# Kernel tuning notes

Measured on AMD Instinct MI355X. Metric: run time of the kernel, lower is better.

Reference implementation:

```python
import jax, jax.numpy as jnp
import numpy as np
import math

D = 1024
H = 16
NEG = -10000.0


def _layernorm(x, g, b, eps=1e-6):
    mu = x.mean(-1, keepdims=True)
    var = ((x - mu) ** 2).mean(-1, keepdims=True)
    return (x - mu) / jnp.sqrt(var + eps) * g + b


def _gelu(x):
    return x * 0.5 * (1.0 + jax.lax.erf(x / math.sqrt(2.0)))


def _split_heads(x):
    N, L, _ = x.shape
    return x.reshape(N, L, H, D // H).transpose(0, 2, 1, 3)  # (N,H,L,d)


def _attention(q, k, v, mask):
    # q,k,v: (N,Lq/Lk,D); mask: (N,1,Lq,Lk) of 0/1 or None
    d = D // H
    qh, kh, vh = _split_heads(q), _split_heads(k), _split_heads(v)
    scores = jnp.einsum('bhqd,bhkd->bhqk', qh, kh) / math.sqrt(d)
    if mask is not None:
        scores = scores + (1.0 - mask) * NEG
    probs = jax.nn.softmax(scores, axis=-1)
    ctx = jnp.einsum('bhqk,bhkd->bhqd', probs, vh)
    N, _, Lq, _ = ctx.shape
    ctx = ctx.transpose(0, 2, 1, 3).reshape(N, Lq, D)
    return ctx, scores.mean(1)  # attention_vis = masked scaled scores averaged over heads


def setup_inputs() -> dict:
    key = jax.random.key(0)
    ks = jax.random.split(key, 16)
    N, Lt, Lv = 16, 512, 512
    w = lambda k: (jax.random.normal(k, (D, D), jnp.float32) * 0.02)
    inp = {
        'dec_hidden_states': jax.random.normal(ks[0], (N, Lt, D), jnp.float32),
        'dec_mask': jnp.ones((N, Lt), jnp.float32),
        'enc_outputs': jax.random.normal(ks[1], (N, Lv, D), jnp.float32),
        'sa_wq': w(ks[2]), 'sa_bq': jnp.zeros((D,), jnp.float32),
        'sa_wk': w(ks[3]), 'sa_bk': jnp.zeros((D,), jnp.float32),
        'sa_wv': w(ks[4]), 'sa_bv': jnp.zeros((D,), jnp.float32),
        'n1_g': jnp.ones((D,), jnp.float32), 'n1_b': jnp.zeros((D,), jnp.float32),
        'ca_wq': w(ks[5]), 'ca_bq': jnp.zeros((D,), jnp.float32),
        'ca_wk': w(ks[6]), 'ca_bk': jnp.zeros((D,), jnp.float32),
        'ca_wv': w(ks[7]), 'ca_bv': jnp.zeros((D,), jnp.float32),
        'n2_g': jnp.ones((D,), jnp.float32), 'n2_b': jnp.zeros((D,), jnp.float32),
        'int_w': w(ks[8]), 'int_b': jnp.zeros((D,), jnp.float32),
        'out_w': w(ks[9]), 'out_b': jnp.zeros((D,), jnp.float32),
        'out_g': jnp.ones((D,), jnp.float32), 'out_beta': jnp.zeros((D,), jnp.float32),
    }
    return inp


def reference(dec_hidden_states, dec_mask, enc_outputs,
              sa_wq, sa_bq, sa_wk, sa_bk, sa_wv, sa_bv, n1_g, n1_b,
              ca_wq, ca_bq, ca_wk, ca_bk, ca_wv, ca_bv, n2_g, n2_b,
              int_w, int_b, out_w, out_b, out_g, out_beta):
    x = dec_hidden_states
    N, Lt, _ = x.shape
    # causal + padding mask: (N,1,Lt) * tril(Lt,Lt) -> (N,Lt,Lt) -> (N,1,Lt,Lt)
    causal = jnp.tril(jnp.ones((Lt, Lt), x.dtype))
    self_mask = (dec_mask[:, None, :] * causal)[:, None, :, :]
    # self attention
    q = x @ sa_wq + sa_bq
    k = x @ sa_wk + sa_bk
    v = x @ sa_wv + sa_bv
    sa_ctx, _ = _attention(q, k, v, self_mask)
    h = _layernorm(sa_ctx + x, n1_g, n1_b)
    # cross attention (no mask)
    cq = h @ ca_wq + ca_bq
    ck = enc_outputs @ ca_wk + ca_bk
    cv = enc_outputs @ ca_wv + ca_bv
    ca_ctx, attention_vis = _attention(cq, ck, cv, None)
    h2 = _layernorm(h + ca_ctx, n2_g, n2_b)
    # intermediate (gelu FFN)
    inter = _gelu(h2 @ int_w + int_b)
    # Output: dense + residual(intermediate itself, as in original) + LayerNorm
    out = _layernorm(inter @ out_w + out_b + inter, out_g, out_beta)
    return out, attention_vis
```

## Files before the change

### kernel.cpp

```cpp
#include <hip/hip_runtime.h>
#include <hip/hip_bf16.h>
#include <math.h>

#define DDIM 1024
#define NH   16
#define LTOK 512
#define NBATCH 16

typedef unsigned short u16;
typedef unsigned short u16x8 __attribute__((ext_vector_type(8)));
typedef unsigned short u16x4 __attribute__((ext_vector_type(4)));
typedef __bf16 bf16x8 __attribute__((ext_vector_type(8)));
typedef float f32x4 __attribute__((ext_vector_type(4)));

typedef __attribute__((address_space(1))) void as1_void;
typedef __attribute__((address_space(3))) void as3_void;

__device__ __forceinline__ void llds16(const u16* g, u16* l) {
    __builtin_amdgcn_global_load_lds((as1_void*)g, (as3_void*)l, 16, 0, 0);
}

__device__ __forceinline__ float bf2f(u16 u) {
    unsigned v = ((unsigned)u) << 16;
    float f; __builtin_memcpy(&f, &v, 4); return f;
}
__device__ __forceinline__ u16 f2bf(float f) {
    unsigned u; __builtin_memcpy(&u, &f, 4);
    u += 0x7fffu + ((u >> 16) & 1u);
    return (u16)(u >> 16);
}

struct GemmOp {
    const u16* A; const u16* B; u16* C; float* Cf; const float* bias;
    u16* VTp;
    long sA1, sA2, sB1, sB2, sC1, sC2;
    int lda, ldb, ldc, M, N, K, zdiv, flags, nblk, vtcol0;
    float scale;
};

template<int MODE>
__global__ __launch_bounds__(256) void gemm_bt_kernel(GemmOp o1, GemmOp o2)
{
    constexpr int NB   = (MODE == 0) ? 1 : 2;
    constexpr int BUFE = 128 * 32;
    __shared__ __align__(16) u16 As[NB * BUFE];
    __shared__ __align__(16) u16 Bs[NB * BUFE];

    const bool second = (int)blockIdx.x >= o1.nblk;
    const GemmOp& o = second ? o2 : o1;
    int bidx = blockIdx.x - (second ? o1.nblk : 0);

    const int tilesN = o.N >> 7;
    const int tilesM = o.M >> 7;
    const int tiles  = tilesM * tilesN;
    const int z = bidx / tiles;
    const int t = bidx - z * tiles;
    const int zb = z / o.zdiv, zh = z - zb * o.zdiv;

    int tm, tn;
    if ((tilesM & 7) == 0) {
        const int xcd = t & 7, idx = t >> 3;
        const int mg  = tilesM >> 3;
        tm = ((idx % mg) << 3) | xcd;
        tn = idx / mg;
    } else {
        tm = t / tilesN;
        tn = t - tm * tilesN;
    }
    const int m0 = tm << 7, n0 = tn << 7;

    const u16* Ab = o.A + (long)zb * o.sA1 + (long)zh * o.sA2;
    const u16* Bb = o.B + (long)zb * o.sB1 + (long)zh * o.sB2;
    u16*   Cb  = o.C  ? o.C  + (long)zb * o.sC1 + (long)zh * o.sC2 : nullptr;
    float* Cfb = o.Cf ? o.Cf + (long)zb * o.sC1 + (long)zh * o.sC2 : nullptr;

    const int tid  = threadIdx.x;
    const int lane = tid & 63;
    const int wave = tid >> 6;
    const int wm = (wave & 1) << 6, wn = (wave >> 1) << 6;
    const int quad = lane >> 4, l16 = lane & 15;

    f32x4 acc[4][4];
#pragma unroll
    for (int i = 0; i < 4; i++)
#pragma unroll
        for (int j = 0; j < 4; j++) acc[i][j] = (f32x4){0.f, 0.f, 0.f, 0.f};

    const int lrA = (wave << 5) + (lane >> 2);
    const int lc  = (((lane & 3) ^ ((lane >> 3) & 3)) << 3);
    const u16* gA0 = Ab + (long)(m0 + lrA) * o.lda + lc;
    const u16* gA1 = Ab + (long)(m0 + lrA + 16) * o.lda + lc;
    const u16* gB0 = Bb + (long)(n0 + lrA) * o.ldb + lc;
    const u16* gB1 = Bb + (long)(n0 + lrA + 16) * o.ldb + lc;
    u16* lA0 = As + ((wave << 5) +  0) * 32;
    u16* lA1 = As + ((wave << 5) + 16) * 32;
    u16* lB0 = Bs + ((wave << 5) +  0) * 32;
    u16* lB1 = Bs + ((wave << 5) + 16) * 32;

    auto STAGE = [&](int bi, int k0) {
        llds16(gA0 + k0, lA0 + bi * BUFE);
        llds16(gA1 + k0, lA1 + bi * BUFE);
        llds16(gB0 + k0, lB0 + bi * BUFE);
        llds16(gB1 + k0, lB1 + bi * BUFE);
    };
    const int cadj = ((l16 >> 1) & 3) << 3;
    auto COMPUTE = [&](int bi) {
        const u16* Ac = As + bi * BUFE;
        const u16* Bc = Bs + bi * BUFE;
        bf16x8 af[4], bfr[4];
#pragma unroll
        for (int t2 = 0; t2 < 4; t2++)
            af[t2] = *(const bf16x8*)(Ac + (wm + t2 * 16 + l16) * 32
                                         + ((quad * 8) ^ cadj));
#pragma unroll
        for (int t2 = 0; t2 < 4; t2++)
            bfr[t2] = *(const bf16x8*)(Bc + (wn + t2 * 16 + l16) * 32
                                          + ((quad * 8) ^ cadj));
#pragma unroll
        for (int i = 0; i < 4; i++)
#pragma unroll
            for (int j = 0; j < 4; j++)
                acc[i][j] = __builtin_amdgcn_mfma_f32_16x16x32_bf16(
                    bfr[j], af[i], acc[i][j], 0, 0, 0);
    };

    const int K = o.K;
    if (MODE == 0) {
        for (int k0 = 0; k0 < K; k0 += 32) {
            __syncthreads();
            STAGE(0, k0);
            __syncthreads();
            COMPUTE(0);
        }
    } else {
        STAGE(0, 0);
        __syncthreads();
        int cur = 0;
        for (int k0 = 0; k0 < K; k0 += 32) {
            const int nxt = cur ^ 1;
            if (k0 + 32 < K) STAGE(nxt, k0 + 32);
            COMPUTE(cur);
            __syncthreads();
            cur = nxt;
        }
    }

#pragma unroll
    for (int i = 0; i < 4; i++) {
        const long row = m0 + wm + i * 16 + l16;
#pragma unroll
        for (int j = 0; j < 4; j++) {
            const int col = n0 + wn + j * 16 + quad * 4;
            f32x4 bv = o.bias ? *(const f32x4*)(o.bias + col)
                              : (f32x4){0.f, 0.f, 0.f, 0.f};
            f32x4 v4;
#pragma unroll
            for (int r = 0; r < 4; r++) {
                float v = acc[i][j][r] * o.scale + bv[r];
                if (o.flags & 1)
                    v = 0.5f * v * (1.f + erff(v * 0.70710678118654752f));
                v4[r] = v;
            }
            if (o.VTp && col >= o.vtcol0) {
                const int dv  = col - o.vtcol0;
                const long bh = (row >> 9) * NH + (dv >> 6);
                const int tok = (int)(row & (LTOK - 1));
                u16* vp = o.VTp + (bh * 64 + (dv & 63)) * LTOK + tok;
#pragma unroll
                for (int r = 0; r < 4; r++)
                    vp[(long)r * LTOK] = f2bf(v4[r]);
            } else if (Cfb) {
                *(f32x4*)(Cfb + row * o.ldc + col) = v4;
            } else {
                u16x4 ov;
#pragma unroll
                for (int r = 0; r < 4; r++) ov[r] = f2bf(v4[r]);
                *(u16x4*)(Cb + row * o.ldc + col) = ov;
            }
        }
    }
}

__global__ __launch_bounds__(256, 2) void flash_kernel(
    const u16* __restrict__ Q, const u16* __restrict__ K,
    const u16* __restrict__ VT, u16* __restrict__ O,
    const float* __restrict__ mask, int causal, int ldq, int ldk)
{
    __shared__ __align__(16) u16 Ks[128 * 72];
    __shared__ __align__(16) u16 Vs[64 * 136];
    const int tid  = threadIdx.x;
    const int wave = tid >> 6, lane = tid & 63;
    const int quad = lane >> 4, l16 = lane & 15;
    const int bh = blockIdx.x, qt = blockIdx.y, b = bh >> 4, h = bh & 15;
    const int qbase = qt * 128 + wave * 32;
    const int qrow0 = qbase + l16;
    const int qrow1 = qbase + 16 + l16;

    const u16* qp0 = Q + ((long)b * LTOK + qrow0) * ldq + h * 64 + quad * 8;
    const u16* qp1 = qp0 + (long)16 * ldq;
    bf16x8 aq00 = *(const bf16x8*)(qp0);
    bf16x8 aq01 = *(const bf16x8*)(qp0 + 32);
    bf16x8 aq10 = *(const bf16x8*)(qp1);
    bf16x8 aq11 = *(const bf16x8*)(qp1 + 32);

    f32x4 oacc0[4], oacc1[4];
#pragma unroll
    for (int jd = 0; jd < 4; jd++) {
        oacc0[jd] = (f32x4){0.f, 0.f, 0.f, 0.f};
        oacc1[jd] = (f32x4){0.f, 0.f, 0.f, 0.f};
    }
    float m0_ = -3.0e38f, m1_ = -3.0e38f;
    float l0_ = 0.f, l1_ = 0.f;

    const int krow = tid >> 3,       kcol = (tid & 7) << 3;
    const int vrow = tid >> 2,       vcol = (tid & 3) << 3;
    const u16* gK = K + ((long)b * LTOK + krow) * ldk + h * 64 + kcol;
    const u16* gV = VT + ((long)bh * 64 + vrow) * LTOK + vcol;

    const float C1    = 0.125f * 1.44269504088896340736f;
    const float NEGL2 = -10000.0f * 1.44269504088896340736f;

    const int nkt = causal ? (qt + 1) : (LTOK >> 7);

    u16x8 KR[4], VR[4];
#pragma unroll
    for (int i = 0; i < 4; i++) KR[i] = *(const u16x8*)(gK + (long)(i * 32) * ldk);
#pragma unroll
    for (int i = 0; i < 4; i++) VR[i] = *(const u16x8*)(gV + i * 32);
#pragma unroll
    for (int i = 0; i < 4; i++)
        *(u16x8*)(Ks + (i * 32 + krow) * 72 + kcol) = KR[i];
#pragma unroll
    for (int i = 0; i < 4; i++)
        *(u16x8*)(Vs + vrow * 136 + i * 32 + vcol) = VR[i];
    __syncthreads();

    for (int kt = 0; kt < nkt; kt++) {
        const int k0 = kt << 7;
        const bool more = (kt + 1 < nkt);

        if (more) {
            const int kn = k0 + 128;
#pragma unroll
            for (int i = 0; i < 4; i++)
                KR[i] = *(const u16x8*)(gK + (long)(kn + i * 32) * ldk);
#pragma unroll
            for (int i = 0; i < 4; i++)
                VR[i] = *(const u16x8*)(gV + kn + i * 32);
        }

        f32x4 s0[8], s1[8];
#pragma unroll
        for (int j = 0; j < 8; j++) {
            bf16x8 bk0 = *(const bf16x8*)(Ks + (j * 16 + l16) * 72 + quad * 8);
            bf16x8 bk1 = *(const bf16x8*)(Ks + (j * 16 + l16) * 72 + 32 + quad * 8);
            f32x4 z0 = (f32x4){0.f, 0.f, 0.f, 0.f};
            z0 = __builtin_amdgcn_mfma_f32_16x16x32_bf16(bk0, aq00, z0, 0, 0, 0);
            s0[j] = __builtin_amdgcn_mfma_f32_16x16x32_bf16(bk1, aq01, z0, 0, 0, 0);
            f32x4 z1 = (f32x4){0.f, 0.f, 0.f, 0.f};
            z1 = __builtin_amdgcn_mfma_f32_16x16x32_bf16(bk0, aq10, z1, 0, 0, 0);
            s1[j] = __builtin_amdgcn_mfma_f32_16x16x32_bf16(bk1, aq11, z1, 0, 0, 0);
        }

        float ta0 = -3.0e38f, ta1 = -3.0e38f, ta2 = -3.0e38f, ta3 = -3.0e38f;
        float tb0 = -3.0e38f, tb1 = -3.0e38f, tb2 = -3.0e38f, tb3 = -3.0e38f;
#pragma unroll
        for (int j = 0; j < 8; j++) {
            if (causal) {
                f32x4 m4 = *(const f32x4*)(mask + (long)b * LTOK + k0 + j * 16 + quad * 4);
#pragma unroll
                for (int r = 0; r < 4; r++) {
                    int key = k0 + j * 16 + quad * 4 + r;
                    float adm = fmaf(m4[r], -NEGL2, NEGL2);
                    s0[j][r] = fmaf(s0[j][r], C1, (key <= qrow0) ? adm : NEGL2);
                    s1[j][r] = fmaf(s1[j][r], C1, (key <= qrow1) ? adm : NEGL2);
                }
            } else {
#pragma unroll
                for (int r = 0; r < 4; r++) { s0[j][r] *= C1; s1[j][r] *= C1; }
            }
            ta0 = fmaxf(ta0, s0[j][0]); ta1 = fmaxf(ta1, s0[j][1]);
            ta2 = fmaxf(ta2, s0[j][2]); ta3 = fmaxf(ta3, s0[j][3]);
            tb0 = fmaxf(tb0, s1[j][0]); tb1 = fmaxf(tb1, s1[j][1]);
            tb2 = fmaxf(tb2, s1[j][2]); tb3 = fmaxf(tb3, s1[j][3]);
        }
        float tmax0 = fmaxf(fmaxf(ta0, ta1), fmaxf(ta2, ta3));
        float tmax1 = fmaxf(fmaxf(tb0, tb1), fmaxf(tb2, tb3));
        tmax0 = fmaxf(tmax0, __shfl_xor(tmax0, 16));
        tmax0 = fmaxf(tmax0, __shfl_xor(tmax0, 32));
        tmax1 = fmaxf(tmax1, __shfl_xor(tmax1, 16));
        tmax1 = fmaxf(tmax1, __shfl_xor(tmax1, 32));

        float mn0 = fmaxf(m0_, tmax0);
        float mn1 = fmaxf(m1_, tmax1);
        float al0 = __builtin_amdgcn_exp2f(m0_ - mn0);
        float al1 = __builtin_amdgcn_exp2f(m1_ - mn1);
        m0_ = mn0; m1_ = mn1;

        unsigned pk0[8][2], pk1[8][2];
        float ra0 = 0.f, ra1 = 0.f, ra2 = 0.f, ra3 = 0.f;
#pragma unroll
        for (int j = 0; j < 8; j++) {
            float p0 = __builtin_amdgcn_exp2f(s0[j][0] - mn0);
            float p1 = __builtin_amdgcn_exp2f(s0[j][1] - mn0);
            float p2 = __builtin_amdgcn_exp2f(s0[j][2] - mn0);
            float p3 = __builtin_amdgcn_exp2f(s0[j][3] - mn0);
            ra0 += p0; ra1 += p1; ra2 += p2; ra3 += p3;
            asm("v_cvt_pk_bf16_f32 %0, %1, %2" : "=v"(pk0[j][0]) : "v"(p0), "v"(p1));
            asm("v_cvt_pk_bf16_f32 %0, %1, %2" : "=v"(pk0[j][1]) : "v"(p2), "v"(p3));
        }
        float rsum0 = (ra0 + ra1) + (ra2 + ra3);
        float rb0 = 0.f, rb1 = 0.f, rb2 = 0.f, rb3 = 0.f;
#pragma unroll
        for (int j = 0; j < 8; j++) {
            float p0 = __builtin_amdgcn_exp2f(s1[j][0] - mn1);
            float p1 = __builtin_amdgcn_exp2f(s1[j][1] - mn1);
            float p2 = __builtin_amdgcn_exp2f(s1[j][2] - mn1);
            float p3 = __builtin_amdgcn_exp2f(s1[j][3] - mn1);
            rb0 += p0; rb1 += p1; rb2 += p2; rb3 += p3;
            asm("v_cvt_pk_bf16_f32 %0, %1, %2" : "=v"(pk1[j][0]) : "v"(p0), "v"(p1));
            asm("v_cvt_pk_bf16_f32 %0, %1, %2" : "=v"(pk1[j][1]) : "v"(p2), "v"(p3));
        }
        float rsum1 = (rb0 + rb1) + (rb2 + rb3);
        rsum0 += __shfl_xor(rsum0, 16);
        rsum0 += __shfl_xor(rsum0, 32);
        rsum1 += __shfl_xor(rsum1, 16);
        rsum1 += __shfl_xor(rsum1, 32);
        l0_ = l0_ * al0 + rsum0;
        l1_ = l1_ * al1 + rsum1;

#pragma unroll
        for (int jd = 0; jd < 4; jd++) { oacc0[jd] *= al0; oacc1[jd] *= al1; }

#pragma unroll
        for (int kk = 0; kk < 4; kk++) {
            unsigned wv0[4] = { pk0[2 * kk][0], pk0[2 * kk][1],
                                pk0[2 * kk + 1][0], pk0[2 * kk + 1][1] };
            unsigned wv1[4] = { pk1[2 * kk][0], pk1[2 * kk][1],
                                pk1[2 * kk + 1][0], pk1[2 * kk + 1][1] };
            bf16x8 bp0; __builtin_memcpy(&bp0, wv0, 16);
            bf16x8 bp1; __builtin_memcpy(&bp1, wv1, 16);
#pragma unroll
            for (int jd = 0; jd < 4; jd++) {
                const u16* vb = Vs + (jd * 16 + l16) * 136 + kk * 32 + quad * 4;
                u16 va[8];
                *(u16x4*)(va)     = *(const u16x4*)(vb);
                *(u16x4*)(va + 4) = *(const u16x4*)(vb + 16);
                bf16x8 av; __builtin_memcpy(&av, va, 16);
                oacc0[jd] = __builtin_amdgcn_mfma_f32_16x16x32_bf16(av, bp0, oacc0[jd], 0, 0, 0);
                oacc1[jd] = __builtin_amdgcn_mfma_f32_16x16x32_bf16(av, bp1, oacc1[jd], 0, 0, 0);
            }
        }

        if (more) {
            __syncthreads();
#pragma unroll
            for (int i = 0; i < 4; i++)
                *(u16x8*)(Ks + (i * 32 + krow) * 72 + kcol) = KR[i];
#pragma unroll
            for (int i = 0; i < 4; i++)
                *(u16x8*)(Vs + vrow * 136 + i * 32 + vcol) = VR[i];
            __syncthreads();
        }
    }

    float li0 = 1.f / l0_;
    float li1 = 1.f / l1_;
    long obase0 = ((long)b * LTOK + qrow0) * DDIM + h * 64;
    long obase1 = obase0 + (long)16 * DDIM;
#pragma unroll
    for (int jd = 0; jd < 4; jd++) {
        u16x4 ov0, ov1;
#pragma unroll
        for (int r = 0; r < 4; r++) {
            ov0[r] = f2bf(oacc0[jd][r] * li0);
            ov1[r] = f2bf(oacc1[jd][r] * li1);
        }
        *(u16x4*)(O + obase0 + jd * 16 + quad * 4) = ov0;
        *(u16x4*)(O + obase1 + jd * 16 + quad * 4) = ov1;
    }
}

__global__ __launch_bounds__(256) void add_ln_kernel(
    const u16* __restrict__ a, const u16* __restrict__ b,
    const float* __restrict__ b32,
    const float* __restrict__ g, const float* __restrict__ bt,
    u16* __restrict__ o, float* __restrict__ of)
{
    long row = blockIdx.x;
    int tid = threadIdx.x;
    __shared__ float red[4];
    const u16* ar = a + row * DDIM;
    float xv[4]; float s = 0.f;
#pragma unroll
    for (int i = 0; i < 4; i++) {
        int c = tid + 256 * i;
        float sum = bf2f(ar[c]) + (b32 ? b32[row * DDIM + c] : bf2f(b[row * DDIM + c]));
        xv[i] = fminf(fmaxf(sum, -1.0e18f), 1.0e18f);
        s += xv[i];
    }
#pragma unroll
    for (int ofs = 32; ofs >= 1; ofs >>= 1) s += __shfl_xor(s, ofs);
    int wave = tid >> 6, lane = tid & 63;
    if (lane == 0) red[wave] = s;
    __syncthreads();
    float mu = (red[0] + red[1] + red[2] + red[3]) * (1.f / 1024.f);
    __syncthreads();
    float v = 0.f;
#pragma unroll
    for (int i = 0; i < 4; i++) { float d = xv[i] - mu; v += d * d; }
#pragma unroll
    for (int ofs = 32; ofs >= 1; ofs >>= 1) v += __shfl_xor(v, ofs);
    if (lane == 0) red[wave] = v;
    __syncthreads();
    float var = (red[0] + red[1] + red[2] + red[3]) * (1.f / 1024.f);
    float inv = rsqrtf(var + 1e-6f);
#pragma unroll
    for (int i = 0; i < 4; i++) {
        int c = tid + 256 * i;
        float r = (xv[i] - mu) * inv * g[c] + bt[c];
        if (of) of[row * DDIM + c] = r;
        else    o [row * DDIM + c] = f2bf(r);
    }
}

__global__ __launch_bounds__(256) void cvt2_kernel(
    const float* __restrict__ s0, u16* __restrict__ d0,
    const float* __restrict__ s1, u16* __restrict__ d1)
{
    const float* src = blockIdx.y ? s1 : s0;
    u16* dst = blockIdx.y ? d1 : d0;
    long i = ((long)blockIdx.x * 256 + threadIdx.x) * 8;
    u16x8 o;
#pragma unroll
    for (int j = 0; j < 8; j++) o[j] = f2bf(src[i + j]);
    *(u16x8*)(dst + i) = o;
}

__global__ __launch_bounds__(256) void wt_kernel(
    const float* w0, const float* w1, const float* w2, const float* w3,
    const float* w4, const float* w5, const float* w6, const float* w7,
    u16* __restrict__ wt)
{
    const float* srcs[8] = {w0, w1, w2, w3, w4, w5, w6, w7};
    const float* w = srcs[blockIdx.z];
    u16* o = wt + (long)blockIdx.z * DDIM * DDIM;
    __shared__ u16 t[32][33];
    int tx = threadIdx.x & 31, ty = threadIdx.x >> 5;
    int c0 = blockIdx.x << 5, r0 = blockIdx.y << 5;
#pragma unroll
    for (int i = 0; i < 4; i++)
        t[ty + 8 * i][tx] = f2bf(w[(long)(r0 + ty + 8 * i) * DDIM + c0 + tx]);
    __syncthreads();
#pragma unroll
    for (int i = 0; i < 4; i++)
        o[(long)(c0 + ty + 8 * i) * DDIM + r0 + tx] = t[tx][ty + 8 * i];
}

__global__ __launch_bounds__(256) void biascat_kernel(
    const float* __restrict__ b0, const float* __restrict__ b1,
    const float* __restrict__ b2, float* __restrict__ dst)
{
    int i = blockIdx.x * 256 + threadIdx.x;
    const float* s = (i < 1024) ? b0 : (i < 2048) ? b1 : b2;
    dst[i] = s[i & 1023];
}

extern "C" void kernel_launch(void* const* d_in, const int* in_sizes, int n_in,
                              void* d_out, int out_size, void* d_ws, size_t ws_size,
                              hipStream_t stream)
{
    const float* x     = (const float*)d_in[0];
    const float* dmsk  = (const float*)d_in[1];
    const float* enc   = (const float*)d_in[2];
    const float* sa_wq = (const float*)d_in[3];  const float* sa_bq = (const float*)d_in[4];
    const float* sa_wk = (const float*)d_in[5];  const float* sa_bk = (const float*)d_in[6];
    const float* sa_wv = (const float*)d_in[7];  const float* sa_bv = (const float*)d_in[8];
    const float* n1_g  = (const float*)d_in[9];  const float* n1_b  = (const float*)d_in[10];
    const float* ca_wq = (const float*)d_in[11]; const float* ca_bq = (const float*)d_in[12];
    const float* ca_wk = (const float*)d_in[13]; const float* ca_bk = (const float*)d_in[14];
    const float* ca_wv = (const float*)d_in[15]; const float* ca_bv = (const float*)d_in[16];
    const float* n2_g  = (const float*)d_in[17]; const float* n2_b  = (const float*)d_in[18];
    const float* int_w = (const float*)d_in[19]; const float* int_b = (const float*)d_in[20];
    const float* out_w = (const float*)d_in[21]; const float* out_b = (const float*)d_in[22];
    const float* out_g = (const float*)d_in[23]; const float* out_bt= (const float*)d_in[24];

    float* outp = (float*)d_out;
    float* visp = outp + (long)NBATCH * LTOK * DDIM;

    const size_t WTB  = (size_t)8 * DDIM * DDIM * 2;
    const size_t BUF1 = (size_t)LTOK * DDIM * 2;
    int cb = 16;
    while (cb > 1 && WTB + (size_t)cb * 7 * BUF1 + 32768 > ws_size)
        cb >>= 1;

    char* ws = (char*)d_ws;
    size_t off = 0;
    auto alloc = [&](size_t bytes) -> u16* {
        u16* p = (u16*)(ws + off);
        off += (bytes + 255) & ~(size_t)255;
        return p;
    };
    u16* Xb  = alloc((size_t)cb * BUF1);
    u16* Eb  = alloc((size_t)cb * BUF1);
    u16* Q3  = alloc((size_t)cb * 3 * BUF1);
    u16* Vt  = alloc((size_t)cb * BUF1);
    u16* Cx  = alloc((size_t)cb * BUF1);
    u16* WT  = alloc(WTB);
    float* biasQKV = (float*)alloc(3072 * sizeof(float));
    float* biasKV  = (float*)alloc(2048 * sizeof(float));

    u16* Wsaq = WT + 0L * DDIM * DDIM;
    u16* Wcaq = WT + 3L * DDIM * DDIM;
    u16* Wcak = WT + 4L * DDIM * DDIM;
    u16* Wint = WT + 6L * DDIM * DDIM;
    u16* Wout = WT + 7L * DDIM * DDIM;

    auto mkop = [](const u16* A, int lda, const u16* B, int ldb,
                   u16* C, float* Cf, int ldc, int M, int N, int K,
                   const float* bias, float scale, int flags) -> GemmOp {
        GemmOp o{};
        o.A = A; o.B = B; o.C = C; o.Cf = Cf; o.bias = bias;
        o.VTp = nullptr; o.vtcol0 = 0;
        o.sA1 = 0; o.sA2 = 0; o.sB1 = 0; o.sB2 = 0; o.sC1 = 0; o.sC2 = 0;
        o.lda = lda; o.ldb = ldb; o.ldc = ldc; o.M = M; o.N = N; o.K = K;
        o.zdiv = 1; o.flags = flags; o.nblk = (M / 128) * (N / 128);
        o.scale = scale;
        return o;
    };

    auto launch = [&](GemmOp o1, GemmOp o2) {
        int nb = o1.nblk + o2.nblk;
        gemm_bt_kernel<1><<<dim3(nb), dim3(256), 0, stream>>>(o1, o2);
    };
    GemmOp nil{};

    const long SLD = (long)LTOK * DDIM;
    const long SSC = (long)LTOK * LTOK;

    wt_kernel<<<dim3(32, 32, 8), dim3(256), 0, stream>>>(
        sa_wq, sa_wk, sa_wv, ca_wq, ca_wk, ca_wv, int_w, out_w, WT);
    biascat_kernel<<<dim3(12), dim3(256), 0, stream>>>(sa_bq, sa_bk, sa_bv, biasQKV);
    biascat_kernel<<<dim3(8),  dim3(256), 0, stream>>>(ca_bk, ca_bv, ca_bv, biasKV);

    for (int b0 = 0; b0 < NBATCH; b0 += cb) {
        const float* xc = x   + (long)b0 * SLD;
        const float* ec = enc + (long)b0 * SLD;
        const int M = cb * LTOK;
        const int Z = cb * NH;
        const int cvtg = (int)(((long)M * DDIM) / (256 * 8));

        u16* h   = Xb;
        u16* CQ  = Q3;
        u16* CKV = Q3 + (size_t)cb * LTOK * DDIM;
        u16* I   = Vt;
        u16* G   = Cx;
        u16* h2  = Eb;

        cvt2_kernel<<<dim3(cvtg, 2), dim3(256), 0, stream>>>(xc, Xb, ec, Eb);

        {
            GemmOp o = mkop(Xb, DDIM, Wsaq, DDIM, Q3, nullptr, 3 * DDIM,
                            M, 3 * DDIM, DDIM, biasQKV, 1.f, 0);
            o.VTp = Vt; o.vtcol0 = 2 * DDIM;
            launch(o, nil);
        }

        flash_kernel<<<dim3(Z, 4), dim3(256), 0, stream>>>(
            Q3, Q3 + DDIM, Vt, Cx, dmsk + (long)b0 * LTOK, 1, 3 * DDIM, 3 * DDIM);

        add_ln_kernel<<<dim3(M), dim3(256), 0, stream>>>(
            Cx, nullptr, xc, n1_g, n1_b, h, nullptr);

        {
            GemmOp okv = mkop(Eb, DDIM, Wcak, DDIM, CKV, nullptr, 2 * DDIM,
                              M, 2 * DDIM, DDIM, biasKV, 1.f, 0);
            okv.VTp = Vt; okv.vtcol0 = DDIM;
            launch(mkop(h, DDIM, Wcaq, DDIM, CQ, nullptr, DDIM,
                        M, DDIM, DDIM, ca_bq, 1.f, 0), okv);
        }

        flash_kernel<<<dim3(Z, 4), dim3(256), 0, stream>>>(
            CQ, CKV, Vt, Cx, nullptr, 0, DDIM, 2 * DDIM);

        add_ln_kernel<<<dim3(M), dim3(256), 0, stream>>>(
            h, Cx, nullptr, n2_g, n2_b, h2, nullptr);

        GemmOp ovis{};
        ovis.A = CQ;  ovis.lda = DDIM;     ovis.sA1 = SLD;               ovis.sA2 = 0;
        ovis.B = CKV; ovis.ldb = 2 * DDIM; ovis.sB1 = (long)LTOK * 2 * DDIM; ovis.sB2 = 0;
        ovis.C = nullptr; ovis.Cf = visp + (long)b0 * SSC;
        ovis.VTp = nullptr; ovis.vtcol0 = 0;
        ovis.ldc = LTOK; ovis.sC1 = SSC; ovis.sC2 = 0;
        ovis.M = LTOK; ovis.N = LTOK; ovis.K = DDIM; ovis.zdiv = 1;
        ovis.bias = nullptr; ovis.scale = 1.f / 128.f; ovis.flags = 0;
        ovis.nblk = (LTOK / 128) * (LTOK / 128) * cb;
        launch(ovis,
               mkop(h2, DDIM, Wint, DDIM, I, nullptr, DDIM,
                    M, DDIM, DDIM, int_b, 1.f, 1));

        launch(mkop(I, DDIM, Wout, DDIM, G, nullptr, DDIM,
                    M, DDIM, DDIM, out_b, 1.f, 0), nil);

        add_ln_kernel<<<dim3(M), dim3(256), 0, stream>>>(
            G, I, nullptr, out_g, out_bt, nullptr, outp + (long)b0 * SLD);
    }
}
```

Before: 533.9 us.

## Add 256x256-tile 8-wave GEMM kernel for QKV and cross-attention projections

Adds a new GEMM kernel using 512 threads, 256x256 output tiles with K-step 64, direct global-to-LDS loads, fine-grained vmcnt waits and barriers interleaved with MFMA phases, and s_setprio around the math. It is used for the self-attention QKV projection and the fused cross-attention Q/KV launch, with the intent of raising operand reuse and overlapping loads with compute. The epilogue is factored into a shared helper, and the old kernel loses its unused single-buffer mode. The larger tiles mean fewer blocks, which risks tail imbalance and lower occupancy from register and LDS pressure.

```diff
diff --git a/kernel.cpp b/kernel.cpp
--- a/kernel.cpp
+++ b/kernel.cpp
@@ -38,13 +38,184 @@
     float scale;
 };
 
-template<int MODE>
+__device__ __forceinline__ void store_frag(
+    const GemmOp& o, u16* Cb, float* Cfb, long row, int col, f32x4 a)
+{
+    f32x4 bv = o.bias ? *(const f32x4*)(o.bias + col)
+                      : (f32x4){0.f, 0.f, 0.f, 0.f};
+    f32x4 v4;
+#pragma unroll
+    for (int r = 0; r < 4; r++) {
+        float v = a[r] * o.scale + bv[r];
+        if (o.flags & 1)
+            v = 0.5f * v * (1.f + erff(v * 0.70710678118654752f));
+        v4[r] = v;
+    }
+    if (o.VTp && col >= o.vtcol0) {
+        const int dv  = col - o.vtcol0;
+        const long bh = (row >> 9) * NH + (dv >> 6);
+        const int tok = (int)(row & (LTOK - 1));
+        u16* vp = o.VTp + (bh * 64 + (dv & 63)) * LTOK + tok;
+#pragma unroll
+        for (int r = 0; r < 4; r++)
+            vp[(long)r * LTOK] = f2bf(v4[r]);
+    } else if (Cfb) {
+        *(f32x4*)(Cfb + row * o.ldc + col) = v4;
+    } else {
+        u16x4 ov;
+#pragma unroll
+        for (int r = 0; r < 4; r++) ov[r] = f2bf(v4[r]);
+        *(u16x4*)(Cb + row * o.ldc + col) = ov;
+    }
+}
+
+__global__ __launch_bounds__(512, 2) void gemm8_kernel(GemmOp o1, GemmOp o2)
+{
+    constexpr int BUFE = 256 * 64;
+    __shared__ __align__(16) u16 As[2 * BUFE];
+    __shared__ __align__(16) u16 Bs[2 * BUFE];
+
+    const bool second = (int)blockIdx.x >= o1.nblk;
+    const GemmOp& o = second ? o2 : o1;
+    int bidx = blockIdx.x - (second ? o1.nblk : 0);
+
+    const int tilesN = o.N >> 8;
+    const int tilesM = o.M >> 8;
+    const int tiles  = tilesM * tilesN;
+    const int z = bidx / tiles;
+    const int t = bidx - z * tiles;
+    const int zb = z / o.zdiv, zh = z - zb * o.zdiv;
+
+    int tm, tn;
+    if ((tilesM & 7) == 0) {
+        const int xcd = t & 7, idx = t >> 3;
+        const int mg  = tilesM >> 3;
+        tm = ((idx % mg) << 3) | xcd;
+        tn = idx / mg;
+    } else {
+        tm = t / tilesN;
+        tn = t - tm * tilesN;
+    }
+    const int m0 = tm << 8, n0 = tn << 8;
+
+    const u16* Ab = o.A + (long)zb * o.sA1 + (long)zh * o.sA2;
+    const u16* Bb = o.B + (long)zb * o.sB1 + (long)zh * o.sB2;
+    u16*   Cb  = o.C  ? o.C  + (long)zb * o.sC1 + (long)zh * o.sC2 : nullptr;
+    float* Cfb = o.Cf ? o.Cf + (long)zb * o.sC1 + (long)zh * o.sC2 : nullptr;
+
+    const int tid  = threadIdx.x;
+    const int lane = tid & 63;
+    const int wave = tid >> 6;
+    const int wm2 = wave >> 2, wn4 = wave & 3;
+    const int quad = lane >> 4, l16 = lane & 15;
+
+    f32x4 acc[8][4];
+#pragma unroll
+    for (int i = 0; i < 8; i++)
+#pragma unroll
+        for (int j = 0; j < 4; j++) acc[i][j] = (f32x4){0.f, 0.f, 0.f, 0.f};
+
+    const int srow  = tid >> 3;
+    const int scol  = (((tid & 7) ^ (srow & 7)) << 3);
+    const u16* gA = Ab + (long)(m0 + srow) * o.lda + scol;
+    const u16* gB = Bb + (long)(n0 + srow) * o.ldb + scol;
+    u16* lA = As + tid * 8;
+    u16* lB = Bs + tid * 8;
+
+    const long ldaL = o.lda, ldbL = o.ldb;
+    auto SA = [&](int par, int k0, int hz) {
+        llds16(gA + (long)(hz * 128) * ldaL + k0,      lA + par * BUFE + hz * 8192);
+        llds16(gA + (long)(hz * 128 + 64) * ldaL + k0, lA + par * BUFE + hz * 8192 + 4096);
+    };
+    auto SB = [&](int par, int k0, int hz) {
+        llds16(gB + (long)(hz * 128) * ldbL + k0,      lB + par * BUFE + hz * 8192);
+        llds16(gB + (long)(hz * 128 + 64) * ldbL + k0, lB + par * BUFE + hz * 8192 + 4096);
+    };
+
+    const int c0 = ((quad)     ^ (l16 & 7)) << 3;
+    const int c1 = ((4 + quad) ^ (l16 & 7)) << 3;
+    const int arow0 = wm2 * 16 + l16;
+    const int brow0 = wn4 * 16 + l16;
+
+    bf16x8 af[4][2], b01[2][2], b23[2][2];
+
+#define LD_A(Ac, mh) do { _Pragma("unroll") \
+    for (int mq2 = 0; mq2 < 4; mq2++) { \
+        const u16* p_ = (Ac) + ((mh) * 128 + mq2 * 32 + arow0) * 64; \
+        af[mq2][0] = *(const bf16x8*)(p_ + c0); \
+        af[mq2][1] = *(const bf16x8*)(p_ + c1); } } while (0)
+#define LD_B(Bc, arr, nh) do { _Pragma("unroll") \
+    for (int nq2 = 0; nq2 < 2; nq2++) { \
+        const u16* p_ = (Bc) + ((nh) * 128 + nq2 * 64 + brow0) * 64; \
+        arr[nq2][0] = *(const bf16x8*)(p_ + c0); \
+        arr[nq2][1] = *(const bf16x8*)(p_ + c1); } } while (0)
+#define MM(arr, mh, nh) do { \
+    __builtin_amdgcn_s_setprio(1); \
+    _Pragma("unroll") for (int mq2 = 0; mq2 < 4; mq2++) \
+    _Pragma("unroll") for (int nq2 = 0; nq2 < 2; nq2++) \
+    _Pragma("unroll") for (int ks = 0; ks < 2; ks++) \
+        acc[(mh)*4 + mq2][(nh)*2 + nq2] = __builtin_amdgcn_mfma_f32_16x16x32_bf16( \
+            arr[nq2][ks], af[mq2][ks], acc[(mh)*4 + mq2][(nh)*2 + nq2], 0, 0, 0); \
+    __builtin_amdgcn_s_setprio(0); } while (0)
+
+    SA(0, 0, 0); SB(0, 0, 0); SB(0, 0, 1); SA(0, 0, 1);
+
+    const int NT = o.K >> 6;
+    for (int k = 0; k < NT; k++) {
+        const int par = k & 1, ip = par ^ 1;
+        const u16* Ac = As + par * BUFE;
+        const u16* Bc = Bs + par * BUFE;
+        const int kn = (k + 1) << 6;
+        const bool more = (k + 1 < NT);
+
+        asm volatile("s_waitcnt vmcnt(4)" ::: "memory");
+        __builtin_amdgcn_s_barrier();
+        asm volatile("" ::: "memory");
+        if (more) SA(ip, kn, 0);
+        LD_A(Ac, 0);
+        LD_B(Bc, b01, 0);
+        MM(b01, 0, 0);
+
+        if (more) asm volatile("s_waitcnt vmcnt(4)" ::: "memory");
+        else      asm volatile("s_waitcnt vmcnt(2)" ::: "memory");
+        __builtin_amdgcn_s_barrier();
+        asm volatile("" ::: "memory");
+        if (more) SB(ip, kn, 0);
+        LD_B(Bc, b23, 1);
+        MM(b23, 0, 1);
+
+        if (more) asm volatile("s_waitcnt vmcnt(4)" ::: "memory");
+        else      asm volatile("s_waitcnt vmcnt(0)" ::: "memory");
+        __builtin_amdgcn_s_barrier();
+        asm volatile("" ::: "memory");
+        if (more) SB(ip, kn, 1);
+        LD_A(Ac, 1);
+        MM(b01, 1, 0);
+
+        if (more) SA(ip, kn, 1);
+        MM(b23, 1, 1);
+    }
+#undef LD_A
+#undef LD_B
+#undef MM
+
+#pragma unroll
+    for (int mq = 0; mq < 8; mq++) {
+        const long row = m0 + (mq >> 2) * 128 + (mq & 3) * 32 + wm2 * 16 + l16;
+#pragma unroll
+        for (int nq = 0; nq < 4; nq++) {
+            const int col = n0 + (nq >> 1) * 128 + (nq & 1) * 64
+                          + wn4 * 16 + quad * 4;
+            store_frag(o, Cb, Cfb, row, col, acc[mq][nq]);
+        }
+    }
+}
+
 __global__ __launch_bounds__(256) void gemm_bt_kernel(GemmOp o1, GemmOp o2)
 {
-    constexpr int NB   = (MODE == 0) ? 1 : 2;
     constexpr int BUFE = 128 * 32;
-    __shared__ __align__(16) u16 As[NB * BUFE];
-    __shared__ __align__(16) u16 Bs[NB * BUFE];
+    __shared__ __align__(16) u16 As[2 * BUFE];
+    __shared__ __align__(16) u16 Bs[2 * BUFE];
 
     const bool second = (int)blockIdx.x >= o1.nblk;
     const GemmOp& o = second ? o2 : o1;
@@ -125,24 +296,15 @@
     };
 
     const int K = o.K;
-    if (MODE == 0) {
-        for (int k0 = 0; k0 < K; k0 += 32) {
-            __syncthreads();
-            STAGE(0, k0);
-            __syncthreads();
-            COMPUTE(0);
-        }
-    } else {
-        STAGE(0, 0);
+    STAGE(0, 0);
+    __syncthreads();
+    int cur = 0;
+    for (int k0 = 0; k0 < K; k0 += 32) {
+        const int nxt = cur ^ 1;
+        if (k0 + 32 < K) STAGE(nxt, k0 + 32);
+        COMPUTE(cur);
         __syncthreads();
-        int cur = 0;
-        for (int k0 = 0; k0 < K; k0 += 32) {
-            const int nxt = cur ^ 1;
-            if (k0 + 32 < K) STAGE(nxt, k0 + 32);
-            COMPUTE(cur);
-            __syncthreads();
-            cur = nxt;
-        }
+        cur = nxt;
     }
 
 #pragma unroll
@@ -151,32 +313,7 @@
 #pragma unroll
         for (int j = 0; j < 4; j++) {
             const int col = n0 + wn + j * 16 + quad * 4;
-            f32x4 bv = o.bias ? *(const f32x4*)(o.bias + col)
-                              : (f32x4){0.f, 0.f, 0.f, 0.f};
-            f32x4 v4;
-#pragma unroll
-            for (int r = 0; r < 4; r++) {
-                float v = acc[i][j][r] * o.scale + bv[r];
-                if (o.flags & 1)
-                    v = 0.5f * v * (1.f + erff(v * 0.70710678118654752f));
-                v4[r] = v;
-            }
-            if (o.VTp && col >= o.vtcol0) {
-                const int dv  = col - o.vtcol0;
-                const long bh = (row >> 9) * NH + (dv >> 6);
-                const int tok = (int)(row & (LTOK - 1));
-                u16* vp = o.VTp + (bh * 64 + (dv & 63)) * LTOK + tok;
-#pragma unroll
-                for (int r = 0; r < 4; r++)
-                    vp[(long)r * LTOK] = f2bf(v4[r]);
-            } else if (Cfb) {
-                *(f32x4*)(Cfb + row * o.ldc + col) = v4;
-            } else {
-                u16x4 ov;
-#pragma unroll
-                for (int r = 0; r < 4; r++) ov[r] = f2bf(v4[r]);
-                *(u16x4*)(Cb + row * o.ldc + col) = ov;
-            }
+            store_frag(o, Cb, Cfb, row, col, acc[i][j]);
         }
     }
 }
@@ -518,20 +655,22 @@
 
     auto mkop = [](const u16* A, int lda, const u16* B, int ldb,
                    u16* C, float* Cf, int ldc, int M, int N, int K,
-                   const float* bias, float scale, int flags) -> GemmOp {
+                   const float* bias, float scale, int flags, int tile) -> GemmOp {
         GemmOp o{};
         o.A = A; o.B = B; o.C = C; o.Cf = Cf; o.bias = bias;
         o.VTp = nullptr; o.vtcol0 = 0;
         o.sA1 = 0; o.sA2 = 0; o.sB1 = 0; o.sB2 = 0; o.sC1 = 0; o.sC2 = 0;
         o.lda = lda; o.ldb = ldb; o.ldc = ldc; o.M = M; o.N = N; o.K = K;
-        o.zdiv = 1; o.flags = flags; o.nblk = (M / 128) * (N / 128);
+        o.zdiv = 1; o.flags = flags; o.nblk = (M / tile) * (N / tile);
         o.scale = scale;
         return o;
     };
 
-    auto launch = [&](GemmOp o1, GemmOp o2) {
-        int nb = o1.nblk + o2.nblk;
-        gemm_bt_kernel<1><<<dim3(nb), dim3(256), 0, stream>>>(o1, o2);
+    auto launch1 = [&](GemmOp o1, GemmOp o2) {
+        gemm_bt_kernel<<<dim3(o1.nblk + o2.nblk), dim3(256), 0, stream>>>(o1, o2);
+    };
+    auto launch8 = [&](GemmOp o1, GemmOp o2) {
+        gemm8_kernel<<<dim3(o1.nblk + o2.nblk), dim3(512), 0, stream>>>(o1, o2);
     };
     GemmOp nil{};
 
@@ -561,9 +700,9 @@
 
         {
             GemmOp o = mkop(Xb, DDIM, Wsaq, DDIM, Q3, nullptr, 3 * DDIM,
-                            M, 3 * DDIM, DDIM, biasQKV, 1.f, 0);
+                            M, 3 * DDIM, DDIM, biasQKV, 1.f, 0, 256);
             o.VTp = Vt; o.vtcol0 = 2 * DDIM;
-            launch(o, nil);
+            launch8(o, nil);
         }
 
         flash_kernel<<<dim3(Z, 4), dim3(256), 0, stream>>>(
@@ -574,10 +713,10 @@
 
         {
             GemmOp okv = mkop(Eb, DDIM, Wcak, DDIM, CKV, nullptr, 2 * DDIM,
-                              M, 2 * DDIM, DDIM, biasKV, 1.f, 0);
+                              M, 2 * DDIM, DDIM, biasKV, 1.f, 0, 256);
             okv.VTp = Vt; okv.vtcol0 = DDIM;
-            launch(mkop(h, DDIM, Wcaq, DDIM, CQ, nullptr, DDIM,
-                        M, DDIM, DDIM, ca_bq, 1.f, 0), okv);
+            launch8(mkop(h, DDIM, Wcaq, DDIM, CQ, nullptr, DDIM,
+                         M, DDIM, DDIM, ca_bq, 1.f, 0, 256), okv);
         }
 
         flash_kernel<<<dim3(Z, 4), dim3(256), 0, stream>>>(
@@ -595,12 +734,12 @@
         ovis.M = LTOK; ovis.N = LTOK; ovis.K = DDIM; ovis.zdiv = 1;
         ovis.bias = nullptr; ovis.scale = 1.f / 128.f; ovis.flags = 0;
         ovis.nblk = (LTOK / 128) * (LTOK / 128) * cb;
-        launch(ovis,
-               mkop(h2, DDIM, Wint, DDIM, I, nullptr, DDIM,
-                    M, DDIM, DDIM, int_b, 1.f, 1));
-
-        launch(mkop(I, DDIM, Wout, DDIM, G, nullptr, DDIM,
-                    M, DDIM, DDIM, out_b, 1.f, 0), nil);
+        launch1(ovis,
+                mkop(h2, DDIM, Wint, DDIM, I, nullptr, DDIM,
+                     M, DDIM, DDIM, int_b, 1.f, 1, 128));
+
+        launch1(mkop(I, DDIM, Wout, DDIM, G, nullptr, DDIM,
+                     M, DDIM, DDIM, out_b, 1.f, 0, 128), nil);
 
         add_ln_kernel<<<dim3(M), dim3(256), 0, stream>>>(
             G, I, nullptr, out_g, out_bt, nullptr, outp + (long)b0 * SLD);
```

Result: slower. 590.6 us (+10.6%).
